# Performance work log

Hardware: AMD Instinct MI355X
Metric: run time of the kernel (lower is better)

The kernel has to match this reference:

```python
import jax, jax.numpy as jnp
import numpy as np

BLKQ = 64
BLKK = 64
TOPK_RATIO = 0.25
EPS = 1e-05


def mean_pool(x, blk):
    B, H, L, D = x.shape
    return x.reshape(B, H, L // blk, blk, D).mean(axis=3)


def setup_inputs() -> dict:
    key = jax.random.key(0)
    kq, kk, kv, kw, kb = jax.random.split(key, 5)
    B, H, Lq, Lk, D = 1, 8, 4096, 4096, 64
    q = jax.random.normal(kq, (B, H, Lq, D), dtype=jnp.float32)
    k = jax.random.normal(kk, (B, H, Lk, D), dtype=jnp.float32)
    v = jax.random.normal(kv, (B, H, Lk, D), dtype=jnp.float32)
    # proj_l is zero-initialized in the original; use small random weights so the
    # linear-attention branch contributes non-trivially to the output.
    proj_w = jax.random.normal(kw, (D, D), dtype=jnp.float32) * 0.02
    proj_b = jax.random.normal(kb, (D,), dtype=jnp.float32) * 0.02
    return {"q": q, "k": k, "v": v, "proj_w": proj_w, "proj_b": proj_b}


def reference(q, k, v, proj_w, proj_b):
    B, H, Lq, D = q.shape
    Lk = k.shape[2]
    nQ, nK = Lq // BLKQ, Lk // BLKK

    # ---- block-level top-k routing (get_block_map_cross) ----
    arg_k = k - k.mean(axis=-2, keepdims=True)
    pq = mean_pool(q, BLKQ)                      # (B,H,nQ,D)
    pk = mean_pool(arg_k, BLKK)                  # (B,H,nK,D)
    pooled_score = jnp.einsum('bhqd,bhkd->bhqk', pq, pk)  # (B,H,nQ,nK)
    topk = min(nK, max(1, int(TOPK_RATIO * nK)))
    lut = jax.lax.top_k(pooled_score, topk)[1]   # (B,H,nQ,topk) int32

    # ---- block-sparse cross attention (softmax over selected K blocks) ----
    qb = q.reshape(B, H, nQ, BLKQ, D)
    kb = k.reshape(B, H, nK, BLKK, D)
    vb = v.reshape(B, H, nK, BLKK, D)
    gather = jax.vmap(jax.vmap(lambda blocks, idx: blocks[idx]))  # over B,H
    kg = gather(kb, lut)                         # (B,H,nQ,topk,BLKK,D)
    vg = gather(vb, lut)                         # (B,H,nQ,topk,BLKK,D)
    scale = D ** -0.5
    s = jnp.einsum('bhnqd,bhntkd->bhnqtk', qb, kg) * scale
    s = s.reshape(B, H, nQ, BLKQ, topk * BLKK)
    p = jax.nn.softmax(s, axis=-1)
    o_s = jnp.einsum('bhnqt,bhntd->bhnqd', p, vg.reshape(B, H, nQ, topk * BLKK, D))
    o_s = o_s.reshape(B, H, Lq, D)

    # ---- linear attention branch (softmax feature map, tied q/k) ----
    qf = jax.nn.softmax(q, axis=-1)
    kf = jax.nn.softmax(k, axis=-1)
    kv = jnp.einsum('bhkd,bhke->bhde', kf, v)    # (B,H,D,D)
    denom = jnp.einsum('bhqd,bhd->bhq', qf, kf.sum(axis=2)) + EPS
    o_l = jnp.einsum('bhqd,bhde->bhqe', qf, kv) / denom[..., None]
    o_l = o_l @ proj_w.T + proj_b                # proj_l

    return o_s + o_l
```

## Files before the change

### kernel.cpp

```cpp
#include <hip/hip_runtime.h>
#include <math.h>

#define H 8
#define L 4096
#define D 64
#define NBLK 64
#define TOPK 16
#define EPS 1e-5f
#define LP 68

typedef unsigned short u16;
typedef unsigned int u32;
typedef __attribute__((ext_vector_type(8))) short bf16x8;
typedef __attribute__((ext_vector_type(16))) float f32x16;
typedef __attribute__((ext_vector_type(4))) u32 u32x4;

static __device__ __forceinline__ u16 f2bf(float x) {
  u32 u = __float_as_uint(x);
  u32 r = (u + 0x7fffu + ((u >> 16) & 1u)) >> 16;
  return (u16)r;
}
static __device__ __forceinline__ float bf2f(u16 h) {
  return __uint_as_float(((u32)h) << 16);
}
__device__ __forceinline__ float dot4f(float4 a, float4 b) {
  return a.x * b.x + a.y * b.y + a.z * b.z + a.w * b.w;
}
static __device__ __forceinline__ void async_cp16(uint4* lds, const uint4* g) {
  __builtin_amdgcn_global_load_lds(
      (const __attribute__((address_space(1))) void*)g,
      (__attribute__((address_space(3))) void*)lds, 16, 0, 0);
}

__global__ __launch_bounds__(256) void kvprep_kernel(
    const float* __restrict__ k, const float* __restrict__ v,
    u16* __restrict__ kpkb, u16* __restrict__ vpkb,
    float* __restrict__ pkp, float* __restrict__ part_kv,
    float* __restrict__ part_ks) {
  const int kb = blockIdx.x, h = blockIdx.y;
  __shared__ float kst[64 * LP];
  __shared__ float vst[64 * LP];
  __shared__ float red[4][64];
  const int t = threadIdx.x;

  {
    const float4* ksrc = (const float4*)(k + ((size_t)h * L + (size_t)kb * 64) * D);
    const float4* vsrc = (const float4*)(v + ((size_t)h * L + (size_t)kb * 64) * D);
#pragma unroll
    for (int i = 0; i < 4; ++i) {
      int flat = i * 256 + t;
      int row = flat >> 4, c4 = flat & 15;
      *(float4*)&kst[row * LP + c4 * 4] = ksrc[flat];
      *(float4*)&vst[row * LP + c4 * 4] = vsrc[flat];
    }
  }
  __syncthreads();

  {
    u16* rowbase = kpkb + ((size_t)h * L + (size_t)kb * 64) * 128;
#pragma unroll
    for (int pass = 0; pass < 2; ++pass) {
      const int key = pass * 32 + (t >> 3);
      const int sub = t & 7;
      float f[8];
#pragma unroll
      for (int e = 0; e < 8; ++e) f[e] = kst[key * LP + sub * 8 + e];
      u16 hi[8], lo[8];
#pragma unroll
      for (int e = 0; e < 8; ++e) {
        hi[e] = f2bf(f[e]);
        lo[e] = f2bf(f[e] - bf2f(hi[e]));
      }
      const int c = sub >> 1, g2 = sub & 1;
      u16* row = rowbase + (size_t)key * 128;
      const int sh = ((c * 4 + g2 * 2 + 0) ^ (key & 15)) * 8;
      const int sl = ((c * 4 + g2 * 2 + 1) ^ (key & 15)) * 8;
      uint4 vh = {(u32)hi[0] | ((u32)hi[1] << 16), (u32)hi[2] | ((u32)hi[3] << 16),
                  (u32)hi[4] | ((u32)hi[5] << 16), (u32)hi[6] | ((u32)hi[7] << 16)};
      uint4 vl = {(u32)lo[0] | ((u32)lo[1] << 16), (u32)lo[2] | ((u32)lo[3] << 16),
                  (u32)lo[4] | ((u32)lo[5] << 16), (u32)lo[6] | ((u32)lo[7] << 16)};
      *(uint4*)(row + sh) = vh;
      *(uint4*)(row + sl) = vl;
    }
  }

  {
    const int d = t & 63, rr = t >> 6;
    float s = 0.f;
#pragma unroll
    for (int i = 0; i < 16; ++i) s += kst[(rr * 16 + i) * LP + d];
    red[rr][d] = s;
  }
  __syncthreads();
  {
    const int d = t & 63, rr = t >> 6;
    if (rr == 0) {
      float tot = red[0][d] + red[1][d] + red[2][d] + red[3][d];
      pkp[((size_t)h * NBLK + kb) * D + d] = tot * (1.f / 64.f);
    }
  }

  {
    u16* base = vpkb + (((size_t)h * 64 + kb) * 64) * 128;
#pragma unroll
    for (int iter = 0; iter < 4; ++iter) {
      const int dim = iter * 16 + (t >> 4);
      const int s = t & 15;
      const int cgh = s ^ (dim & 15);
      const int c = cgh >> 2, g = (cgh >> 1) & 1, hl = cgh & 1;
      u16 o[8];
#pragma unroll
      for (int e = 0; e < 8; ++e) {
        const int key = 4 * g + (e & 3) + 8 * ((e >> 2) + 2 * (c & 1)) + 32 * (c >> 1);
        float val = vst[key * LP + dim];
        u16 hi = f2bf(val);
        o[e] = hl ? f2bf(val - bf2f(hi)) : hi;
      }
      uint4 pk4 = {(u32)o[0] | ((u32)o[1] << 16), (u32)o[2] | ((u32)o[3] << 16),
                   (u32)o[4] | ((u32)o[5] << 16), (u32)o[6] | ((u32)o[7] << 16)};
      *(uint4*)(base + (size_t)dim * 128 + s * 8) = pk4;
    }
  }

  if (t < 128) {
    const int row = t >> 1, half = t & 1;
    float4 kr[8];
#pragma unroll
    for (int i = 0; i < 8; ++i) kr[i] = *(float4*)&kst[row * LP + half * 32 + i * 4];
    float mxk = -INFINITY;
#pragma unroll
    for (int i = 0; i < 8; ++i)
      mxk = fmaxf(mxk, fmaxf(fmaxf(kr[i].x, kr[i].y), fmaxf(kr[i].z, kr[i].w)));
    mxk = fmaxf(mxk, __shfl_xor(mxk, 1));
    float smk = 0.f;
#pragma unroll
    for (int i = 0; i < 8; ++i) {
      kr[i].x = __expf(kr[i].x - mxk); kr[i].y = __expf(kr[i].y - mxk);
      kr[i].z = __expf(kr[i].z - mxk); kr[i].w = __expf(kr[i].w - mxk);
      smk += kr[i].x + kr[i].y + kr[i].z + kr[i].w;
    }
    smk += __shfl_xor(smk, 1);
    const float inv = 1.f / smk;
#pragma unroll
    for (int i = 0; i < 8; ++i) {
      float4 o = kr[i];
      o.x *= inv; o.y *= inv; o.z *= inv; o.w *= inv;
      *(float4*)&kst[row * LP + half * 32 + i * 4] = o;
    }
  }
  __syncthreads();

  {
    const int d = t & 63, eg = t >> 6;
    float4 acc0 = make_float4(0.f, 0.f, 0.f, 0.f);
    float4 acc1 = acc0, acc2 = acc0, acc3 = acc0;
    float ksacc = 0.f;
#pragma unroll 4
    for (int lr = 0; lr < 64; ++lr) {
      const float wv = kst[lr * LP + d];
      if (eg == 0) ksacc += wv;
      const float4* vr = (const float4*)&vst[lr * LP + eg * 16];
      float4 v0 = vr[0], v1 = vr[1], v2 = vr[2], v3 = vr[3];
      acc0.x += wv * v0.x; acc0.y += wv * v0.y; acc0.z += wv * v0.z; acc0.w += wv * v0.w;
      acc1.x += wv * v1.x; acc1.y += wv * v1.y; acc1.z += wv * v1.z; acc1.w += wv * v1.w;
      acc2.x += wv * v2.x; acc2.y += wv * v2.y; acc2.z += wv * v2.z; acc2.w += wv * v2.w;
      acc3.x += wv * v3.x; acc3.y += wv * v3.y; acc3.z += wv * v3.z; acc3.w += wv * v3.w;
    }
    float* kvb = part_kv + ((size_t)(h * 64 + kb)) * 4096 + (size_t)d * 64 + eg * 16;
    *(float4*)(kvb + 0) = acc0;
    *(float4*)(kvb + 4) = acc1;
    *(float4*)(kvb + 8) = acc2;
    *(float4*)(kvb + 12) = acc3;
    if (eg == 0) part_ks[(size_t)(h * 64 + kb) * 64 + d] = ksacc;
  }
}

__global__ __launch_bounds__(256) void pool_kernel(
    const float* __restrict__ src, float* __restrict__ dst) {
  const int blk = blockIdx.x, h = blockIdx.y;
  const int d = threadIdx.x & 63, rr = threadIdx.x >> 6;
  const float* base = src + ((size_t)h * L + (size_t)blk * 64) * D;
  float s = 0.f;
#pragma unroll
  for (int i = 0; i < 16; ++i) s += base[(rr * 16 + i) * D + d];
  __shared__ float red[4][64];
  red[rr][d] = s;
  __syncthreads();
  if (rr == 0) {
    float tot = red[0][d] + red[1][d] + red[2][d] + red[3][d];
    dst[((size_t)h * NBLK + blk) * D + d] = tot * (1.f / 64.f);
  }
}

__global__ __launch_bounds__(64) void topk_kernel(
    const float* __restrict__ pq, const float* __restrict__ pk,
    int* __restrict__ lut) {
  const int qb = blockIdx.x, h = blockIdx.y;
  const int j = threadIdx.x;
  const float4* pqv = (const float4*)(pq + ((size_t)h * NBLK + qb) * D);
  const float4* pkv = (const float4*)(pk + ((size_t)h * NBLK + j) * D);
  float s = 0.f;
#pragma unroll
  for (int d4 = 0; d4 < 16; ++d4) s += dot4f(pqv[d4], pkv[d4]);
  int* lrow = lut + ((size_t)h * NBLK + qb) * TOPK;
  for (int t = 0; t < TOPK; ++t) {
    float m = s;
    int mi = j;
#pragma unroll
    for (int off = 32; off; off >>= 1) {
      float om = __shfl_xor(m, off);
      int omi = __shfl_xor(mi, off);
      if (om > m || (om == m && omi < mi)) { m = om; mi = omi; }
    }
    if (j == 0) lrow[t] = mi;
    if (j == mi) s = -INFINITY;
  }
}

__global__ __launch_bounds__(256, 2) void sattn_kernel(
    const float* __restrict__ q, const u16* __restrict__ kpk,
    const u16* __restrict__ vpk, const int* __restrict__ lut,
    float* __restrict__ out) {
  __shared__ alignas(16) char smem[65536];
  const int bx = blockIdx.x;
  const int h = bx & 7, qb = bx >> 3;
  const int t = threadIdx.x;
  const int lane = t & 63;
  const int ln = lane & 31;
  const int g = lane >> 5;
  const int w = t >> 6;
  const int p = w & 1;
  const int kh = w >> 1;

  bf16x8 qh[4], ql[4];
  {
    const float* qrowp = q + ((size_t)h * L + (size_t)qb * 64 + p * 32 + ln) * D;
#pragma unroll
    for (int c = 0; c < 4; ++c) {
      float4 a = *(const float4*)(qrowp + c * 16 + g * 8);
      float4 b = *(const float4*)(qrowp + c * 16 + g * 8 + 4);
      float f[8] = {a.x, a.y, a.z, a.w, b.x, b.y, b.z, b.w};
#pragma unroll
      for (int e = 0; e < 8; ++e) {
        float x = f[e] * 0.125f;
        u16 hi = f2bf(x);
        qh[c][e] = (short)hi;
        ql[c][e] = (short)f2bf(x - bf2f(hi));
      }
    }
  }

  u16* bufA = (u16*)smem;
  u16* bufB = (u16*)smem + 16384;

  f32x16 o0, o1;
#pragma unroll
  for (int r = 0; r < 16; ++r) { o0[r] = 0.f; o1[r] = 0.f; }
  float lrun = 0.f;
  const int* lrow = lut + ((size_t)h * NBLK + qb) * TOPK;
  const int xr = ln & 15;
  const int krow = kh * 32 + ln;

#define STAGE(dst, kbi)                                                        \
  {                                                                            \
    const int kb_ = (kbi);                                                     \
    const uint4* gk = (const uint4*)(kpk + ((size_t)h * L + (size_t)kb_ * 64) * 128); \
    const uint4* gv = (const uint4*)(vpk + (((size_t)h * 64 + kb_) * 64) * 128);      \
    uint4* lk = (uint4*)(dst);                                                 \
    uint4* lv = (uint4*)((dst) + 8192);                                        \
    _Pragma("unroll") for (int i_ = 0; i_ < 4; ++i_) {                         \
      int x_ = i_ * 256 + t;                                                   \
      async_cp16(lk + x_, gk + x_);                                            \
      async_cp16(lv + x_, gv + x_);                                            \
    }                                                                          \
  }

  STAGE(bufA, lrow[0]);
  __syncthreads();

  u16* cur = bufA;
  u16* nxt = bufB;
  for (int ib = 0; ib < TOPK; ++ib) {
    if (ib + 1 < TOPK) STAGE(nxt, lrow[ib + 1]);

    const u16* KB = cur;
    const u16* VB = cur + 8192;

    f32x16 s0;
#pragma unroll
    for (int r = 0; r < 16; ++r) s0[r] = 0.f;
    __builtin_amdgcn_s_setprio(1);
#pragma unroll
    for (int c = 0; c < 4; ++c) {
      const int sH = c * 4 + g * 2;
      bf16x8 k_h = *(const bf16x8*)(KB + (size_t)krow * 128 + ((sH ^ xr) * 8));
      bf16x8 k_l = *(const bf16x8*)(KB + (size_t)krow * 128 + (((sH + 1) ^ xr) * 8));
      s0 = __builtin_amdgcn_mfma_f32_32x32x16_bf16(k_h, qh[c], s0, 0, 0, 0);
      s0 = __builtin_amdgcn_mfma_f32_32x32x16_bf16(k_l, qh[c], s0, 0, 0, 0);
      s0 = __builtin_amdgcn_mfma_f32_32x32x16_bf16(k_h, ql[c], s0, 0, 0, 0);
    }
    __builtin_amdgcn_s_setprio(0);

    u32 hpk[8], lpk[8];
    float psum = 0.f;
#pragma unroll
    for (int j = 0; j < 8; ++j) {
      float a = __expf(s0[2 * j]);
      float b = __expf(s0[2 * j + 1]);
      psum += a + b;
      u32 hp;
      asm("v_cvt_pk_bf16_f32 %0, %1, %2" : "=v"(hp) : "v"(a), "v"(b));
      hpk[j] = hp;
      float ah = __uint_as_float(hp << 16);
      float bh = __uint_as_float(hp & 0xffff0000u);
      u32 lp;
      asm("v_cvt_pk_bf16_f32 %0, %1, %2" : "=v"(lp) : "v"(a - ah), "v"(b - bh));
      lpk[j] = lp;
    }
    psum += __shfl_xor(psum, 32);
    lrun += psum;

    __builtin_amdgcn_s_setprio(1);
#pragma unroll
    for (int cc = 0; cc < 2; ++cc) {
      union { u32x4 u; bf16x8 b; } ph, pl;
      ph.u = (u32x4){hpk[4 * cc + 0], hpk[4 * cc + 1], hpk[4 * cc + 2], hpk[4 * cc + 3]};
      pl.u = (u32x4){lpk[4 * cc + 0], lpk[4 * cc + 1], lpk[4 * cc + 2], lpk[4 * cc + 3]};
      const bf16x8 pah = ph.b, pal = pl.b;
      const int sH = (2 * kh + cc) * 4 + g * 2;
      bf16x8 v0h = *(const bf16x8*)(VB + (size_t)ln * 128 + ((sH ^ xr) * 8));
      bf16x8 v0l = *(const bf16x8*)(VB + (size_t)ln * 128 + (((sH + 1) ^ xr) * 8));
      bf16x8 v1h = *(const bf16x8*)(VB + (size_t)(32 + ln) * 128 + ((sH ^ xr) * 8));
      bf16x8 v1l = *(const bf16x8*)(VB + (size_t)(32 + ln) * 128 + (((sH + 1) ^ xr) * 8));
      o0 = __builtin_amdgcn_mfma_f32_32x32x16_bf16(pah, v0h, o0, 0, 0, 0);
      o0 = __builtin_amdgcn_mfma_f32_32x32x16_bf16(pal, v0h, o0, 0, 0, 0);
      o0 = __builtin_amdgcn_mfma_f32_32x32x16_bf16(pah, v0l, o0, 0, 0, 0);
      o1 = __builtin_amdgcn_mfma_f32_32x32x16_bf16(pah, v1h, o1, 0, 0, 0);
      o1 = __builtin_amdgcn_mfma_f32_32x32x16_bf16(pal, v1h, o1, 0, 0, 0);
      o1 = __builtin_amdgcn_mfma_f32_32x32x16_bf16(pah, v1l, o1, 0, 0, 0);
    }
    __builtin_amdgcn_s_setprio(0);

    __syncthreads();
    u16* tmp = cur; cur = nxt; nxt = tmp;
  }
#undef STAGE

  float* oxbase = (float*)smem;
  float* lxbase = (float*)smem + 4096;
  if (g == 0) lxbase[(p * 2 + kh) * 32 + ln] = lrun;
  if (kh == 1) {
#pragma unroll
    for (int r = 0; r < 16; ++r) {
      const int R = (r & 3) + 8 * (r >> 2) + 4 * g;
      oxbase[p * 2048 + R * 64 + ln] = o0[r];
      oxbase[p * 2048 + R * 64 + 32 + ln] = o1[r];
    }
  }
  __syncthreads();
  if (kh == 0) {
#pragma unroll
    for (int r = 0; r < 16; ++r) {
      const int R = (r & 3) + 8 * (r >> 2) + 4 * g;
      const float lt = lxbase[(p * 2 + 0) * 32 + R] + lxbase[(p * 2 + 1) * 32 + R];
      const float inv = 1.f / lt;
      const size_t row = (size_t)h * L + (size_t)qb * 64 + p * 32 + R;
      out[row * 64 + ln] = (o0[r] + oxbase[p * 2048 + R * 64 + ln]) * inv;
      out[row * 64 + 32 + ln] = (o1[r] + oxbase[p * 2048 + R * 64 + 32 + ln]) * inv;
    }
  }
}

__global__ __launch_bounds__(256) void kvred_kernel(
    const float* __restrict__ part_kv, const float* __restrict__ part_ks,
    float* __restrict__ p2kv, float* __restrict__ p2ks) {
  const int j = blockIdx.x, h = blockIdx.y;
  const int t = threadIdx.x;
  float4 s0 = make_float4(0.f, 0.f, 0.f, 0.f);
  float4 s1 = s0, s2 = s0, s3 = s0;
#pragma unroll
  for (int p = 0; p < 4; ++p) {
    const float4* src = (const float4*)(part_kv + ((size_t)(h * 64 + j * 4 + p)) * 4096);
    float4 a = src[0 * 256 + t], b = src[1 * 256 + t];
    float4 c = src[2 * 256 + t], d = src[3 * 256 + t];
    s0.x += a.x; s0.y += a.y; s0.z += a.z; s0.w += a.w;
    s1.x += b.x; s1.y += b.y; s1.z += b.z; s1.w += b.w;
    s2.x += c.x; s2.y += c.y; s2.z += c.z; s2.w += c.w;
    s3.x += d.x; s3.y += d.y; s3.z += d.z; s3.w += d.w;
  }
  float4* dst = (float4*)(p2kv + ((size_t)(h * 16 + j)) * 4096);
  dst[0 * 256 + t] = s0;
  dst[1 * 256 + t] = s1;
  dst[2 * 256 + t] = s2;
  dst[3 * 256 + t] = s3;
  if (t < 64) {
    float ks = 0.f;
#pragma unroll
    for (int p = 0; p < 4; ++p) ks += part_ks[(size_t)(h * 64 + j * 4 + p) * 64 + t];
    p2ks[(size_t)(h * 16 + j) * 64 + t] = ks;
  }
}

__global__ __launch_bounds__(256) void kvproj_kernel(
    const float* __restrict__ p2kv, const float* __restrict__ p2ks,
    const float* __restrict__ pw, float* __restrict__ kvp,
    float* __restrict__ ksum) {
  const int h = blockIdx.x;
  __shared__ float kvs[64 * 64];
  __shared__ float pws[64 * 64];
  const int t = threadIdx.x;
  float4 s0 = make_float4(0.f, 0.f, 0.f, 0.f);
  float4 s1 = s0, s2 = s0, s3 = s0;
  for (int p = 0; p < 16; ++p) {
    const float4* src = (const float4*)(p2kv + ((size_t)(h * 16 + p)) * 4096);
    float4 a = src[0 * 256 + t], b = src[1 * 256 + t];
    float4 cc = src[2 * 256 + t], dd = src[3 * 256 + t];
    s0.x += a.x; s0.y += a.y; s0.z += a.z; s0.w += a.w;
    s1.x += b.x; s1.y += b.y; s1.z += b.z; s1.w += b.w;
    s2.x += cc.x; s2.y += cc.y; s2.z += cc.z; s2.w += cc.w;
    s3.x += dd.x; s3.y += dd.y; s3.z += dd.z; s3.w += dd.w;
  }
  ((float4*)kvs)[0 * 256 + t] = s0;
  ((float4*)kvs)[1 * 256 + t] = s1;
  ((float4*)kvs)[2 * 256 + t] = s2;
  ((float4*)kvs)[3 * 256 + t] = s3;
#pragma unroll
  for (int i = 0; i < 4; ++i) {
    int f4 = i * 256 + t;
    ((float4*)pws)[f4] = ((const float4*)pw)[f4];
  }
  if (t < 64) {
    float ks = 0.f;
    for (int p = 0; p < 16; ++p) ks += p2ks[(size_t)(h * 16 + p) * 64 + t];
    ksum[(size_t)h * 64 + t] = ks;
  }
  __syncthreads();
  const int d = t & 63, fg = t >> 6;
  float* dst = kvp + (size_t)h * 4096 + (size_t)d * 64;
  const float4* a = (const float4*)&kvs[d * 64];
  for (int f = fg * 16; f < fg * 16 + 16; ++f) {
    const float4* b = (const float4*)&pws[f * 64];
    float s = 0.f;
#pragma unroll
    for (int e4 = 0; e4 < 16; ++e4) s += dot4f(a[e4], b[e4]);
    dst[f] = s;
  }
}

__global__ __launch_bounds__(256) void linattn_kernel(
    const float* __restrict__ q, const float* __restrict__ kvp,
    const float* __restrict__ ksum, const float* __restrict__ pb,
    float* __restrict__ out) {
  __shared__ float kvs[64 * 64];
  __shared__ float kss[64], pbs[64];
  const int t = threadIdx.x;
  const size_t grow = (size_t)blockIdx.x * 256 + t;
  const int h = (int)(grow >> 12);
#pragma unroll
  for (int i = 0; i < 4; ++i) {
    int f4 = i * 256 + t;
    ((float4*)kvs)[f4] = ((const float4*)(kvp + (size_t)h * 4096))[f4];
  }
  if (t < 64) {
    kss[t] = ksum[(size_t)h * 64 + t];
    pbs[t] = pb[t];
  }
  __syncthreads();
  const float* qrow = q + grow * 64;
  float mx = -INFINITY;
  const float4* q4p = (const float4*)qrow;
#pragma unroll
  for (int i = 0; i < 16; ++i) {
    float4 x = q4p[i];
    mx = fmaxf(mx, fmaxf(fmaxf(x.x, x.y), fmaxf(x.z, x.w)));
  }
  float4 tt[16];
#pragma unroll
  for (int i = 0; i < 16; ++i) tt[i] = make_float4(0.f, 0.f, 0.f, 0.f);
  float sm = 0.f, dn = 0.f;
#pragma unroll 4
  for (int dd = 0; dd < 64; ++dd) {
    const float wv = __expf(qrow[dd] - mx);
    sm += wv;
    dn += wv * kss[dd];
    const float4* kvr = (const float4*)&kvs[dd * 64];
#pragma unroll
    for (int e4 = 0; e4 < 16; ++e4) {
      float4 kk = kvr[e4];
      tt[e4].x += wv * kk.x; tt[e4].y += wv * kk.y;
      tt[e4].z += wv * kk.z; tt[e4].w += wv * kk.w;
    }
  }
  const float inv = 1.f / (dn + EPS * sm);
  float* orow = out + grow * 64;
#pragma unroll
  for (int e4 = 0; e4 < 16; ++e4) {
    float4 o = ((float4*)orow)[e4];
    o.x += tt[e4].x * inv + pbs[e4 * 4 + 0];
    o.y += tt[e4].y * inv + pbs[e4 * 4 + 1];
    o.z += tt[e4].z * inv + pbs[e4 * 4 + 2];
    o.w += tt[e4].w * inv + pbs[e4 * 4 + 3];
    ((float4*)orow)[e4] = o;
  }
}

extern "C" void kernel_launch(void* const* d_in, const int* in_sizes, int n_in,
                              void* d_out, int out_size, void* d_ws, size_t ws_size,
                              hipStream_t stream) {
  const float* q = (const float*)d_in[0];
  const float* k = (const float*)d_in[1];
  const float* v = (const float*)d_in[2];
  const float* pw = (const float*)d_in[3];
  const float* pb = (const float*)d_in[4];
  float* out = (float*)d_out;

  u16* kpkb = (u16*)d_ws;
  u16* vpkb = (u16*)d_ws + 4194304;
  float* fws = (float*)((char*)d_ws + 16777216);
  float* pq = fws;
  float* pk = fws + 32768;
  float* part_kv = fws + 65536;
  float* part_ks = fws + 2162688;
  float* p2kv = fws + 2195456;
  float* p2ks = fws + 2719744;
  float* kvp = fws + 2727936;
  float* ksum = fws + 2760704;
  int* lut = (int*)(fws + 2761216);

  kvprep_kernel<<<dim3(64, 8), 256, 0, stream>>>(k, v, kpkb, vpkb, pk, part_kv, part_ks);
  pool_kernel<<<dim3(64, 8), 256, 0, stream>>>(q, pq);
  topk_kernel<<<dim3(64, 8), 64, 0, stream>>>(pq, pk, lut);
  sattn_kernel<<<512, 256, 0, stream>>>(q, kpkb, vpkb, lut, out);
  kvred_kernel<<<dim3(16, 8), 256, 0, stream>>>(part_kv, part_ks, p2kv, p2ks);
  kvproj_kernel<<<8, 256, 0, stream>>>(p2kv, p2ks, pw, kvp, ksum);
  linattn_kernel<<<128, 256, 0, stream>>>(q, kvp, ksum, pb, out);
}
```

Measured before the change: 172.0 us.

## Fuse pooling into top-k, split sparse attention across two K streams, drop kvred

```diff
diff --git a/kernel.cpp b/kernel.cpp
--- a/kernel.cpp
+++ b/kernel.cpp
@@ -25,11 +25,6 @@
 }
 __device__ __forceinline__ float dot4f(float4 a, float4 b) {
   return a.x * b.x + a.y * b.y + a.z * b.z + a.w * b.w;
-}
-static __device__ __forceinline__ void async_cp16(uint4* lds, const uint4* g) {
-  __builtin_amdgcn_global_load_lds(
-      (const __attribute__((address_space(1))) void*)g,
-      (__attribute__((address_space(3))) void*)lds, 16, 0, 0);
 }
 
 __global__ __launch_bounds__(256) void kvprep_kernel(
@@ -175,49 +170,49 @@
   }
 }
 
-__global__ __launch_bounds__(256) void pool_kernel(
-    const float* __restrict__ src, float* __restrict__ dst) {
-  const int blk = blockIdx.x, h = blockIdx.y;
-  const int d = threadIdx.x & 63, rr = threadIdx.x >> 6;
-  const float* base = src + ((size_t)h * L + (size_t)blk * 64) * D;
-  float s = 0.f;
-#pragma unroll
-  for (int i = 0; i < 16; ++i) s += base[(rr * 16 + i) * D + d];
-  __shared__ float red[4][64];
-  red[rr][d] = s;
-  __syncthreads();
-  if (rr == 0) {
-    float tot = red[0][d] + red[1][d] + red[2][d] + red[3][d];
-    dst[((size_t)h * NBLK + blk) * D + d] = tot * (1.f / 64.f);
-  }
-}
-
-__global__ __launch_bounds__(64) void topk_kernel(
-    const float* __restrict__ pq, const float* __restrict__ pk,
+__global__ __launch_bounds__(256) void topkq_kernel(
+    const float* __restrict__ q, const float* __restrict__ pk,
     int* __restrict__ lut) {
   const int qb = blockIdx.x, h = blockIdx.y;
-  const int j = threadIdx.x;
-  const float4* pqv = (const float4*)(pq + ((size_t)h * NBLK + qb) * D);
-  const float4* pkv = (const float4*)(pk + ((size_t)h * NBLK + j) * D);
-  float s = 0.f;
-#pragma unroll
-  for (int d4 = 0; d4 < 16; ++d4) s += dot4f(pqv[d4], pkv[d4]);
-  int* lrow = lut + ((size_t)h * NBLK + qb) * TOPK;
-  for (int t = 0; t < TOPK; ++t) {
-    float m = s;
-    int mi = j;
-#pragma unroll
-    for (int off = 32; off; off >>= 1) {
-      float om = __shfl_xor(m, off);
-      int omi = __shfl_xor(mi, off);
-      if (om > m || (om == m && omi < mi)) { m = om; mi = omi; }
-    }
-    if (j == 0) lrow[t] = mi;
-    if (j == mi) s = -INFINITY;
-  }
-}
-
-__global__ __launch_bounds__(256, 2) void sattn_kernel(
+  __shared__ float red[4][64];
+  __shared__ alignas(16) float pqv[64];
+  const int t = threadIdx.x;
+  const int d = t & 63, rr = t >> 6;
+  {
+    const float* base = q + ((size_t)h * L + (size_t)qb * 64) * D;
+    float s = 0.f;
+#pragma unroll
+    for (int i = 0; i < 16; ++i) s += base[(rr * 16 + i) * D + d];
+    red[rr][d] = s;
+  }
+  __syncthreads();
+  if (rr == 0)
+    pqv[d] = (red[0][d] + red[1][d] + red[2][d] + red[3][d]) * (1.f / 64.f);
+  __syncthreads();
+  if (t < 64) {
+    const int j = t;
+    const float4* pq4 = (const float4*)pqv;
+    const float4* pk4 = (const float4*)(pk + ((size_t)h * NBLK + j) * D);
+    float sc = 0.f;
+#pragma unroll
+    for (int d4 = 0; d4 < 16; ++d4) sc += dot4f(pq4[d4], pk4[d4]);
+    int* lrow = lut + ((size_t)h * NBLK + qb) * TOPK;
+    for (int it = 0; it < TOPK; ++it) {
+      float m = sc;
+      int mi = j;
+#pragma unroll
+      for (int off = 32; off; off >>= 1) {
+        float om = __shfl_xor(m, off);
+        int omi = __shfl_xor(mi, off);
+        if (om > m || (om == m && omi < mi)) { m = om; mi = omi; }
+      }
+      if (j == 0) lrow[it] = mi;
+      if (j == mi) sc = -INFINITY;
+    }
+  }
+}
+
+__global__ __launch_bounds__(512, 4) void sattn_kernel(
     const float* __restrict__ q, const u16* __restrict__ kpk,
     const u16* __restrict__ vpk, const int* __restrict__ lut,
     float* __restrict__ out) {
@@ -230,7 +225,9 @@
   const int g = lane >> 5;
   const int w = t >> 6;
   const int p = w & 1;
-  const int kh = w >> 1;
+  const int kh = (w >> 1) & 1;
+  const int j = w >> 2;
+  const int th = t & 255;
 
   bf16x8 qh[4], ql[4];
   {
@@ -250,8 +247,10 @@
     }
   }
 
-  u16* bufA = (u16*)smem;
-  u16* bufB = (u16*)smem + 16384;
+  const u16* KB = (const u16*)smem + j * 16384;
+  const u16* VB = KB + 8192;
+  uint4* lk = (uint4*)((u16*)smem + j * 16384);
+  uint4* lv = lk + 1024;
 
   f32x16 o0, o1;
 #pragma unroll
@@ -261,31 +260,31 @@
   const int xr = ln & 15;
   const int krow = kh * 32 + ln;
 
-#define STAGE(dst, kbi)                                                        \
-  {                                                                            \
-    const int kb_ = (kbi);                                                     \
+  uint4 pf[8];
+#define LOADR(ibi)                                                               \
+  {                                                                              \
+    const int kb_ = lrow[2 * (ibi) + j];                                         \
     const uint4* gk = (const uint4*)(kpk + ((size_t)h * L + (size_t)kb_ * 64) * 128); \
     const uint4* gv = (const uint4*)(vpk + (((size_t)h * 64 + kb_) * 64) * 128);      \
-    uint4* lk = (uint4*)(dst);                                                 \
-    uint4* lv = (uint4*)((dst) + 8192);                                        \
-    _Pragma("unroll") for (int i_ = 0; i_ < 4; ++i_) {                         \
-      int x_ = i_ * 256 + t;                                                   \
-      async_cp16(lk + x_, gk + x_);                                            \
-      async_cp16(lv + x_, gv + x_);                                            \
-    }                                                                          \
-  }
-
-  STAGE(bufA, lrow[0]);
-  __syncthreads();
-
-  u16* cur = bufA;
-  u16* nxt = bufB;
-  for (int ib = 0; ib < TOPK; ++ib) {
-    if (ib + 1 < TOPK) STAGE(nxt, lrow[ib + 1]);
-
-    const u16* KB = cur;
-    const u16* VB = cur + 8192;
-
+    _Pragma("unroll") for (int i_ = 0; i_ < 4; ++i_) {                           \
+      pf[i_] = gk[i_ * 256 + th];                                                \
+      pf[4 + i_] = gv[i_ * 256 + th];                                            \
+    }                                                                            \
+  }
+#define WRITES                                                                   \
+  {                                                                              \
+    _Pragma("unroll") for (int i_ = 0; i_ < 4; ++i_) {                           \
+      lk[i_ * 256 + th] = pf[i_];                                                \
+      lv[i_ * 256 + th] = pf[4 + i_];                                            \
+    }                                                                            \
+  }
+
+  LOADR(0);
+  WRITES;
+  LOADR(1);
+  __syncthreads();
+
+  for (int ib = 0; ib < 8; ++ib) {
     f32x16 s0;
 #pragma unroll
     for (int r = 0; r < 16; ++r) s0[r] = 0.f;
@@ -304,18 +303,18 @@
     u32 hpk[8], lpk[8];
     float psum = 0.f;
 #pragma unroll
-    for (int j = 0; j < 8; ++j) {
-      float a = __expf(s0[2 * j]);
-      float b = __expf(s0[2 * j + 1]);
+    for (int jj = 0; jj < 8; ++jj) {
+      float a = __expf(s0[2 * jj]);
+      float b = __expf(s0[2 * jj + 1]);
       psum += a + b;
       u32 hp;
       asm("v_cvt_pk_bf16_f32 %0, %1, %2" : "=v"(hp) : "v"(a), "v"(b));
-      hpk[j] = hp;
+      hpk[jj] = hp;
       float ah = __uint_as_float(hp << 16);
       float bh = __uint_as_float(hp & 0xffff0000u);
       u32 lp;
       asm("v_cvt_pk_bf16_f32 %0, %1, %2" : "=v"(lp) : "v"(a - ah), "v"(b - bh));
-      lpk[j] = lp;
+      lpk[jj] = lp;
     }
     psum += __shfl_xor(psum, 32);
     lrun += psum;
@@ -342,67 +341,49 @@
     __builtin_amdgcn_s_setprio(0);
 
     __syncthreads();
-    u16* tmp = cur; cur = nxt; nxt = tmp;
-  }
-#undef STAGE
-
-  float* oxbase = (float*)smem;
-  float* lxbase = (float*)smem + 4096;
-  if (g == 0) lxbase[(p * 2 + kh) * 32 + ln] = lrun;
-  if (kh == 1) {
+    if (ib + 1 < 8) { WRITES; }
+    if (ib + 2 < 8) LOADR(ib + 2);
+    __syncthreads();
+  }
+#undef LOADR
+#undef WRITES
+
+  float* oxb = (float*)smem;
+  float* lxb = (float*)smem + 12288;
+  __syncthreads();
+  const int cmb = kh + 2 * j;
+  if (g == 0) lxb[(p * 4 + cmb) * 32 + ln] = lrun;
+  if (cmb != 0) {
 #pragma unroll
     for (int r = 0; r < 16; ++r) {
       const int R = (r & 3) + 8 * (r >> 2) + 4 * g;
-      oxbase[p * 2048 + R * 64 + ln] = o0[r];
-      oxbase[p * 2048 + R * 64 + 32 + ln] = o1[r];
-    }
-  }
-  __syncthreads();
-  if (kh == 0) {
+      oxb[(p * 3 + cmb - 1) * 2048 + R * 64 + ln] = o0[r];
+      oxb[(p * 3 + cmb - 1) * 2048 + R * 64 + 32 + ln] = o1[r];
+    }
+  }
+  __syncthreads();
+  if (cmb == 0) {
 #pragma unroll
     for (int r = 0; r < 16; ++r) {
       const int R = (r & 3) + 8 * (r >> 2) + 4 * g;
-      const float lt = lxbase[(p * 2 + 0) * 32 + R] + lxbase[(p * 2 + 1) * 32 + R];
+      const float lt = lxb[(p * 4 + 0) * 32 + R] + lxb[(p * 4 + 1) * 32 + R] +
+                       lxb[(p * 4 + 2) * 32 + R] + lxb[(p * 4 + 3) * 32 + R];
       const float inv = 1.f / lt;
+      float a0 = o0[r], a1 = o1[r];
+#pragma unroll
+      for (int s = 0; s < 3; ++s) {
+        a0 += oxb[(p * 3 + s) * 2048 + R * 64 + ln];
+        a1 += oxb[(p * 3 + s) * 2048 + R * 64 + 32 + ln];
+      }
       const size_t row = (size_t)h * L + (size_t)qb * 64 + p * 32 + R;
-      out[row * 64 + ln] = (o0[r] + oxbase[p * 2048 + R * 64 + ln]) * inv;
-      out[row * 64 + 32 + ln] = (o1[r] + oxbase[p * 2048 + R * 64 + 32 + ln]) * inv;
-    }
-  }
-}
-
-__global__ __launch_bounds__(256) void kvred_kernel(
+      out[row * 64 + ln] = a0 * inv;
+      out[row * 64 + 32 + ln] = a1 * inv;
+    }
+  }
+}
+
+__global__ __launch_bounds__(256) void kvproj_kernel(
     const float* __restrict__ part_kv, const float* __restrict__ part_ks,
-    float* __restrict__ p2kv, float* __restrict__ p2ks) {
-  const int j = blockIdx.x, h = blockIdx.y;
-  const int t = threadIdx.x;
-  float4 s0 = make_float4(0.f, 0.f, 0.f, 0.f);
-  float4 s1 = s0, s2 = s0, s3 = s0;
-#pragma unroll
-  for (int p = 0; p < 4; ++p) {
-    const float4* src = (const float4*)(part_kv + ((size_t)(h * 64 + j * 4 + p)) * 4096);
-    float4 a = src[0 * 256 + t], b = src[1 * 256 + t];
-    float4 c = src[2 * 256 + t], d = src[3 * 256 + t];
-    s0.x += a.x; s0.y += a.y; s0.z += a.z; s0.w += a.w;
-    s1.x += b.x; s1.y += b.y; s1.z += b.z; s1.w += b.w;
-    s2.x += c.x; s2.y += c.y; s2.z += c.z; s2.w += c.w;
-    s3.x += d.x; s3.y += d.y; s3.z += d.z; s3.w += d.w;
-  }
-  float4* dst = (float4*)(p2kv + ((size_t)(h * 16 + j)) * 4096);
-  dst[0 * 256 + t] = s0;
-  dst[1 * 256 + t] = s1;
-  dst[2 * 256 + t] = s2;
-  dst[3 * 256 + t] = s3;
-  if (t < 64) {
-    float ks = 0.f;
-#pragma unroll
-    for (int p = 0; p < 4; ++p) ks += part_ks[(size_t)(h * 64 + j * 4 + p) * 64 + t];
-    p2ks[(size_t)(h * 16 + j) * 64 + t] = ks;
-  }
-}
-
-__global__ __launch_bounds__(256) void kvproj_kernel(
-    const float* __restrict__ p2kv, const float* __restrict__ p2ks,
     const float* __restrict__ pw, float* __restrict__ kvp,
     float* __restrict__ ksum) {
   const int h = blockIdx.x;
@@ -411,8 +392,8 @@
   const int t = threadIdx.x;
   float4 s0 = make_float4(0.f, 0.f, 0.f, 0.f);
   float4 s1 = s0, s2 = s0, s3 = s0;
-  for (int p = 0; p < 16; ++p) {
-    const float4* src = (const float4*)(p2kv + ((size_t)(h * 16 + p)) * 4096);
+  for (int p = 0; p < 64; ++p) {
+    const float4* src = (const float4*)(part_kv + ((size_t)(h * 64 + p)) * 4096);
     float4 a = src[0 * 256 + t], b = src[1 * 256 + t];
     float4 cc = src[2 * 256 + t], dd = src[3 * 256 + t];
     s0.x += a.x; s0.y += a.y; s0.z += a.z; s0.w += a.w;
@@ -431,7 +412,7 @@
   }
   if (t < 64) {
     float ks = 0.f;
-    for (int p = 0; p < 16; ++p) ks += p2ks[(size_t)(h * 16 + p) * 64 + t];
+    for (int p = 0; p < 64; ++p) ks += part_ks[(size_t)(h * 64 + p) * 64 + t];
     ksum[(size_t)h * 64 + t] = ks;
   }
   __syncthreads();
@@ -517,21 +498,16 @@
   u16* kpkb = (u16*)d_ws;
   u16* vpkb = (u16*)d_ws + 4194304;
   float* fws = (float*)((char*)d_ws + 16777216);
-  float* pq = fws;
   float* pk = fws + 32768;
   float* part_kv = fws + 65536;
   float* part_ks = fws + 2162688;
-  float* p2kv = fws + 2195456;
-  float* p2ks = fws + 2719744;
   float* kvp = fws + 2727936;
   float* ksum = fws + 2760704;
   int* lut = (int*)(fws + 2761216);
 
   kvprep_kernel<<<dim3(64, 8), 256, 0, stream>>>(k, v, kpkb, vpkb, pk, part_kv, part_ks);
-  pool_kernel<<<dim3(64, 8), 256, 0, stream>>>(q, pq);
-  topk_kernel<<<dim3(64, 8), 64, 0, stream>>>(pq, pk, lut);
-  sattn_kernel<<<512, 256, 0, stream>>>(q, kpkb, vpkb, lut, out);
-  kvred_kernel<<<dim3(16, 8), 256, 0, stream>>>(part_kv, part_ks, p2kv, p2ks);
-  kvproj_kernel<<<8, 256, 0, stream>>>(p2kv, p2ks, pw, kvp, ksum);
+  topkq_kernel<<<dim3(64, 8), 256, 0, stream>>>(q, pk, lut);
+  sattn_kernel<<<512, 512, 0, stream>>>(q, kpkb, vpkb, lut, out);
+  kvproj_kernel<<<8, 256, 0, stream>>>(part_kv, part_ks, pw, kvp, ksum);
   linattn_kernel<<<128, 256, 0, stream>>>(q, kvp, ksum, pb, out);
 }
```

After: 243.3 us. 1.41x slower.
